# Optimization experiments

Measured on AMD Instinct MI355X. Metric: run time of the kernel, lower is better.

## Reference

```python
import jax, jax.numpy as jnp
import numpy as np

B, S, E, H = 2, 2048, 1024, 16
D = E // H

def setup_inputs() -> dict:
    key = jax.random.key(0)
    ks = jax.random.split(key, 11)
    sc = 0.02
    inp = {
        'queries': jax.random.normal(ks[0], (B, S, E), jnp.float32),
        'keys':    jax.random.normal(ks[1], (B, S, E), jnp.float32),
        'values':  jax.random.normal(ks[2], (B, S, E), jnp.float32),
        'Wq': jax.random.normal(ks[3], (E, E), jnp.float32) * sc,
        'bq': jnp.zeros((E,), jnp.float32),
        'Wk': jax.random.normal(ks[4], (E, E), jnp.float32) * sc,
        'bk': jnp.zeros((E,), jnp.float32),
        'Wv': jax.random.normal(ks[5], (E, E), jnp.float32) * sc,
        'bv': jnp.zeros((E,), jnp.float32),
        'Wo': jax.random.normal(ks[6], (E, E), jnp.float32) * sc,
        'bo': jnp.zeros((E,), jnp.float32),
        'indicator': 0,
    }
    return inp

def reference(queries, keys, values, Wq, bq, Wk, bk, Wv, bv, Wo, bo, indicator):
    # torch Linear: y = x @ W.T + b
    q = queries @ Wq.T + bq
    k = keys    @ Wk.T + bk
    v = values  @ Wv.T + bv
    # [B,S,E] -> [B,H,S,D]
    q = q.reshape(B, S, H, D).transpose(0, 2, 1, 3)
    k = k.reshape(B, S, H, D).transpose(0, 2, 1, 3)
    v = v.reshape(B, S, H, D).transpose(0, 2, 1, 3)
    scores = jnp.einsum('bhqd,bhkd->bhqk', q, k) / jnp.sqrt(jnp.float32(D))
    w = jax.nn.sigmoid(scores)
    if indicator != 0:
        w = 1.0 - w
    attn = jax.nn.softmax(w, axis=-1)  # dropout_prob=0 -> identity
    out = jnp.einsum('bhqk,bhkd->bhqd', attn, v)
    out = out.transpose(0, 2, 1, 3).reshape(B, S, E)
    return out @ Wo.T + bo
```

## Files before the change

kernel.cpp:

```cpp
#include <hip/hip_runtime.h>
#include <stdint.h>

#define Bb 2
#define Ss 2048
#define Ee 1024
#define Hh 16
#define Dd 64

typedef __bf16 bf16;
typedef __attribute__((ext_vector_type(8))) __bf16 bf16x8;
typedef __attribute__((ext_vector_type(4))) __bf16 bf16x4;
typedef __attribute__((ext_vector_type(4))) float f32x4;

#define MB (1u << 20)
#define OFF_XQ 0u
#define OFF_XK (8u * MB)
#define OFF_XV (16u * MB)
#define OFF_WQ (24u * MB)
#define OFF_WK (26u * MB)
#define OFF_WV (28u * MB)
#define OFF_WO (30u * MB)
#define OFF_Q  (32u * MB)
#define OFF_K  (40u * MB)
#define OFF_VT (48u * MB)
#define OFF_AO (56u * MB)

__device__ __forceinline__ void gll16(const void* g, void* lds) {
  __builtin_amdgcn_global_load_lds(
      (const __attribute__((address_space(1))) void*)g,
      (__attribute__((address_space(3))) void*)lds, 16, 0, 0);
}

__device__ __forceinline__ unsigned pkbf(float lo, float hi) {
  unsigned r;
  asm("v_cvt_pk_bf16_f32 %0, %1, %2" : "=v"(r) : "v"(lo), "v"(hi));
  return r;
}
#define PL32SWAP(a, b) asm("v_permlane32_swap_b32 %0, %1" : "+v"(a), "+v"(b))
#define PL16SWAP(a, b) asm("v_permlane16_swap_b32 %0, %1" : "+v"(a), "+v"(b))

__global__ __launch_bounds__(256) void convert_kernel(
    const float* __restrict__ q, const float* __restrict__ k, const float* __restrict__ v,
    const float* __restrict__ wq, const float* __restrict__ wk, const float* __restrict__ wv,
    const float* __restrict__ wo, const int* __restrict__ ind, char* __restrict__ ws)
{
  const unsigned i = blockIdx.x * 256u + threadIdx.x;
  const float* src;
  bf16* dst;
  float scale = 1.0f;
  if (i < 3145728u) {
    const unsigned a = i >> 20, j = i & 1048575u;
    src = (a == 0 ? q : a == 1 ? k : v) + (size_t)j * 4;
    dst = (bf16*)(ws + (size_t)a * (8u * MB)) + (size_t)j * 4;
  } else {
    const unsigned i2 = i - 3145728u;
    const unsigned a = i2 >> 18, j = i2 & 262143u;
    src = (a == 0 ? wq : a == 1 ? wk : a == 2 ? wv : wo) + (size_t)j * 4;
    dst = (bf16*)(ws + OFF_WQ + (size_t)a * (2u * MB)) + (size_t)j * 4;
    if (a == 0) {
      const float c1v = (*ind != 0) ? 1.442695041f : -1.442695041f;
      scale = 0.125f * c1v;
    }
  }
  const float4 f = *(const float4*)src;
  bf16x4 o;
  o[0] = (bf16)(f.x * scale);
  o[1] = (bf16)(f.y * scale);
  o[2] = (bf16)(f.z * scale);
  o[3] = (bf16)(f.w * scale);
  *(bf16x4*)dst = o;
}

__device__ __forceinline__ void gemm128_body(
    const bf16* __restrict__ A, const bf16* __restrict__ W,
    char* smem, int m0, int n0, int t, f32x4 (&acc)[4][4])
{
  char* As = smem;
  char* Bs = smem + 16384;
  const int lane = t & 63;
  const int wid = t >> 6;
  const int wm = (wid >> 1) << 6;
  const int wn = (wid & 1) << 6;
  for (int kt = 0; kt < 1024; kt += 64) {
    __syncthreads();
#pragma unroll
    for (int i = 0; i < 4; ++i) {
      const int L = i * 4096 + t * 16;
      const int r = L >> 7;
      const int c = ((L >> 4) & 7) ^ (r & 7);
      gll16(A + (size_t)(m0 + r) * 1024 + kt + c * 8, As + i * 4096 + wid * 1024);
      gll16(W + (size_t)(n0 + r) * 1024 + kt + c * 8, Bs + i * 4096 + wid * 1024);
    }
    __syncthreads();
#pragma unroll
    for (int ks = 0; ks < 2; ++ks) {
      bf16x8 af[4], bff[4];
#pragma unroll
      for (int mi = 0; mi < 4; ++mi) {
        const int r = wm + mi * 16 + (lane & 15);
        const int c = (ks * 4 + (lane >> 4)) ^ (r & 7);
        af[mi] = *(const bf16x8*)(As + r * 128 + c * 16);
      }
#pragma unroll
      for (int ni = 0; ni < 4; ++ni) {
        const int r = wn + ni * 16 + (lane & 15);
        const int c = (ks * 4 + (lane >> 4)) ^ (r & 7);
        bff[ni] = *(const bf16x8*)(Bs + r * 128 + c * 16);
      }
      __builtin_amdgcn_s_setprio(1);
#pragma unroll
      for (int mi = 0; mi < 4; ++mi)
#pragma unroll
        for (int ni = 0; ni < 4; ++ni)
          acc[mi][ni] = __builtin_amdgcn_mfma_f32_16x16x32_bf16(af[mi], bff[ni], acc[mi][ni], 0, 0, 0);
      __builtin_amdgcn_s_setprio(0);
    }
  }
}

__global__ __launch_bounds__(256) void proj_gemm(
    char* __restrict__ ws, const float* __restrict__ bq,
    const float* __restrict__ bk, const float* __restrict__ bv,
    const int* __restrict__ ind)
{
  __shared__ __align__(16) char smem[32768];
  const int zi = blockIdx.z;
  const bf16* A = (const bf16*)(ws + (zi == 0 ? OFF_XQ : zi == 1 ? OFF_XK : OFF_XV));
  const bf16* W = (const bf16*)(ws + (zi == 0 ? OFF_WQ : zi == 1 ? OFF_WK : OFF_WV));
  const float* bias = zi == 0 ? bq : zi == 1 ? bk : bv;
  bf16* outp = (bf16*)(ws + (zi == 0 ? OFF_Q : zi == 1 ? OFF_K : OFF_VT));
  const float c1v = (*ind != 0) ? 1.442695041f : -1.442695041f;
  const float bscale = (zi == 0) ? 0.125f * c1v : 1.0f;
  const int t = threadIdx.x;
  const int m0 = blockIdx.y * 128, n0 = blockIdx.x * 128;
  f32x4 acc[4][4] = {};
  gemm128_body(A, W, smem, m0, n0, t, acc);
  const int lane = t & 63, wid = t >> 6;
  const int wm = (wid >> 1) << 6, wn = (wid & 1) << 6;
  const int cl = lane & 15, rl = lane >> 4;
#pragma unroll
  for (int ni = 0; ni < 4; ++ni) {
    const int col = n0 + wn + ni * 16 + cl;
    const float bvv = bias[col] * bscale;
    const int h = col >> 6, d = col & 63;
#pragma unroll
    for (int mi = 0; mi < 4; ++mi) {
      const int row0 = m0 + wm + mi * 16 + rl * 4;
      const int b = row0 >> 11, s = row0 & 2047;
      if (zi == 2) {
        bf16x4 o;
#pragma unroll
        for (int r2 = 0; r2 < 4; ++r2) o[r2] = (bf16)(acc[mi][ni][r2] + bvv);
        *(bf16x4*)&outp[((size_t)((b * Hh + h) * Dd + d) * Ss) + s] = o;
      } else {
#pragma unroll
        for (int r2 = 0; r2 < 4; ++r2) {
          const float val = acc[mi][ni][r2] + bvv;
          outp[((size_t)((b * Hh + h) * Ss + s + r2) * Dd) + d] = (bf16)val;
        }
      }
    }
  }
}

__global__ __launch_bounds__(256, 2) void attn_kernel(char* __restrict__ ws)
{
  __shared__ __align__(16) char smem[49152];
  char* Qs  = smem;
  char* Ks  = smem + 16384;
  char* Vts = smem + 32768;
  char* Os  = smem;
  const int t = threadIdx.x, lane = t & 63, wid = t >> 6;
  const int g = lane >> 4, l15 = lane & 15;
  const int bh = blockIdx.y;
  const int q0 = blockIdx.x * 128;
  const bf16* Qg  = (const bf16*)(ws + OFF_Q)  + (size_t)bh * Ss * Dd;
  const bf16* Kg  = (const bf16*)(ws + OFF_K)  + (size_t)bh * Ss * Dd;
  const bf16* Vtg = (const bf16*)(ws + OFF_VT) + (size_t)bh * Ss * Dd;
  bf16* AO = (bf16*)(ws + OFF_AO);

#pragma unroll
  for (int i = 0; i < 4; ++i) {
    const int L = i * 4096 + t * 16;
    const int r = L >> 7;
    const int c = ((L >> 4) & 7) ^ (r & 7);
    gll16(Qg + (size_t)(q0 + r) * Dd + c * 8, Qs + i * 4096 + wid * 1024);
  }
  __syncthreads();
  bf16x8 qf[2][2];
#pragma unroll
  for (int qh = 0; qh < 2; ++qh)
#pragma unroll
    for (int ks = 0; ks < 2; ++ks) {
      const int r = wid * 32 + qh * 16 + l15;
      const int c = (ks * 4 + g) ^ (r & 7);
      qf[qh][ks] = *(const bf16x8*)(Qs + r * 128 + c * 16);
    }

  f32x4 acc_o[2][4] = {};
  f32x4 acc_sum[2] = {};
  union { unsigned u[4]; bf16x8 v; } ones_;
#pragma unroll
  for (int j = 0; j < 4; ++j) ones_.u[j] = 0x3F803F80u;

  for (int kt = 0; kt < Ss; kt += 128) {
    __syncthreads();
#pragma unroll
    for (int i = 0; i < 4; ++i) {
      const int L = i * 4096 + t * 16;
      const int r = L >> 7;
      const int c = ((L >> 4) & 7) ^ (r & 7);
      gll16(Kg + (size_t)(kt + r) * Dd + c * 8, Ks + i * 4096 + wid * 1024);
    }
#pragma unroll
    for (int i = 0; i < 4; ++i) {
      const int L = i * 4096 + t * 16;
      const int r = L >> 8;
      const int c = ((L >> 4) & 15) ^ (r & 15);
      gll16(Vtg + (size_t)r * Ss + kt + c * 8, Vts + i * 4096 + wid * 1024);
    }
    __syncthreads();

    f32x4 st[2][8];
#pragma unroll
    for (int qh = 0; qh < 2; ++qh)
#pragma unroll
      for (int ni = 0; ni < 8; ++ni)
        st[qh][ni] = (f32x4){-0.52876637f, -0.52876637f, -0.52876637f, -0.52876637f};
    __builtin_amdgcn_s_setprio(1);
#pragma unroll
    for (int ks = 0; ks < 2; ++ks) {
#pragma unroll
      for (int ni = 0; ni < 8; ++ni) {
        const int r = ni * 16 + l15;
        const int c = (ks * 4 + g) ^ (r & 7);
        const bf16x8 kf = *(const bf16x8*)(Ks + r * 128 + c * 16);
        st[0][ni] = __builtin_amdgcn_mfma_f32_16x16x32_bf16(kf, qf[0][ks], st[0][ni], 0, 0, 0);
        st[1][ni] = __builtin_amdgcn_mfma_f32_16x16x32_bf16(kf, qf[1][ks], st[1][ni], 0, 0, 0);
      }
    }
    __builtin_amdgcn_s_setprio(0);

#pragma unroll
    for (int kb = 0; kb < 4; ++kb) {
      union { unsigned u[4]; bf16x8 v; } pb[2];
#pragma unroll
      for (int qh = 0; qh < 2; ++qh) {
        float p[2][4];
#pragma unroll
        for (int e = 0; e < 2; ++e)
#pragma unroll
          for (int r2 = 0; r2 < 4; ++r2) {
            const float ex = __builtin_amdgcn_exp2f(st[qh][2 * kb + e][r2]);
            const float tt = __builtin_amdgcn_rcpf(0.69314718f + ex);
            p[e][r2] = __builtin_amdgcn_exp2f(tt);
          }
        unsigned E0 = pkbf(p[0][0], p[0][1]);
        unsigned E1 = pkbf(p[0][2], p[0][3]);
        unsigned O0 = pkbf(p[1][0], p[1][1]);
        unsigned O1 = pkbf(p[1][2], p[1][3]);
        PL32SWAP(E0, O0);
        PL16SWAP(E0, O0);
        PL32SWAP(E1, O1);
        PL16SWAP(E1, O1);
        pb[qh].u[0] = E0; pb[qh].u[1] = E1; pb[qh].u[2] = O0; pb[qh].u[3] = O1;
      }
      __builtin_amdgcn_s_setprio(1);
#pragma unroll
      for (int dblk = 0; dblk < 4; ++dblk) {
        const int r = dblk * 16 + l15;
        const int c = (kb * 4 + g) ^ (r & 15);
        const bf16x8 vf = *(const bf16x8*)(Vts + r * 256 + c * 16);
        acc_o[0][dblk] = __builtin_amdgcn_mfma_f32_16x16x32_bf16(vf, pb[0].v, acc_o[0][dblk], 0, 0, 0);
        acc_o[1][dblk] = __builtin_amdgcn_mfma_f32_16x16x32_bf16(vf, pb[1].v, acc_o[1][dblk], 0, 0, 0);
      }
      acc_sum[0] = __builtin_amdgcn_mfma_f32_16x16x32_bf16(ones_.v, pb[0].v, acc_sum[0], 0, 0, 0);
      acc_sum[1] = __builtin_amdgcn_mfma_f32_16x16x32_bf16(ones_.v, pb[1].v, acc_sum[1], 0, 0, 0);
      __builtin_amdgcn_s_setprio(0);
    }
  }

  const float rinv[2] = {__builtin_amdgcn_rcpf(acc_sum[0][0]),
                         __builtin_amdgcn_rcpf(acc_sum[1][0])};

  __syncthreads();
#pragma unroll
  for (int qh = 0; qh < 2; ++qh) {
    const int row = wid * 32 + qh * 16 + l15;
#pragma unroll
    for (int dblk = 0; dblk < 4; ++dblk) {
      const unsigned w0 = pkbf(acc_o[qh][dblk][0] * rinv[qh], acc_o[qh][dblk][1] * rinv[qh]);
      const unsigned w1 = pkbf(acc_o[qh][dblk][2] * rinv[qh], acc_o[qh][dblk][3] * rinv[qh]);
      const int cc = dblk * 2 + (g >> 1);
      char* a = Os + row * 128 + (cc ^ (row & 7)) * 16 + (g & 1) * 8;
      *(uint2*)a = make_uint2(w0, w1);
    }
  }
  __syncthreads();
  const int b = bh >> 4, h = bh & 15;
#pragma unroll
  for (int i = 0; i < 4; ++i) {
    const int L = i * 4096 + t * 16;
    const int r = L >> 7;
    const int cc = (L >> 4) & 7;
    const uint4 w = *(const uint4*)(Os + r * 128 + (cc ^ (r & 7)) * 16);
    *(uint4*)&AO[((size_t)(b * Ss + q0 + r) << 10) + h * 64 + cc * 8] = w;
  }
}

__global__ __launch_bounds__(256) void out_gemm(char* __restrict__ ws,
                                                const float* __restrict__ bo,
                                                float* __restrict__ outp)
{
  __shared__ __align__(16) char smem[24576];
  char* As = smem;
  char* Bs = smem + 16384;
  const bf16* A = (const bf16*)(ws + OFF_AO);
  const bf16* W = (const bf16*)(ws + OFF_WO);
  const int t = threadIdx.x, lane = t & 63, wid = t >> 6;
  const int l15 = lane & 15, g = lane >> 4;
  const int m0 = blockIdx.y * 128, n0 = blockIdx.x * 64;
  const int wm = (wid >> 1) << 6;
  const int wn = (wid & 1) << 5;
  f32x4 acc[4][2] = {};
  for (int kt = 0; kt < 1024; kt += 64) {
    __syncthreads();
#pragma unroll
    for (int i = 0; i < 4; ++i) {
      const int L = i * 4096 + t * 16;
      const int r = L >> 7;
      const int c = ((L >> 4) & 7) ^ (r & 7);
      gll16(A + (size_t)(m0 + r) * 1024 + kt + c * 8, As + i * 4096 + wid * 1024);
    }
#pragma unroll
    for (int i = 0; i < 2; ++i) {
      const int L = i * 4096 + t * 16;
      const int r = L >> 7;
      const int c = ((L >> 4) & 7) ^ (r & 7);
      gll16(W + (size_t)(n0 + r) * 1024 + kt + c * 8, Bs + i * 4096 + wid * 1024);
    }
    __syncthreads();
#pragma unroll
    for (int ks = 0; ks < 2; ++ks) {
      bf16x8 af[4], bff[2];
#pragma unroll
      for (int mi = 0; mi < 4; ++mi) {
        const int r = wm + mi * 16 + l15;
        const int c = (ks * 4 + g) ^ (r & 7);
        af[mi] = *(const bf16x8*)(As + r * 128 + c * 16);
      }
#pragma unroll
      for (int ni = 0; ni < 2; ++ni) {
        const int r = wn + ni * 16 + l15;
        const int c = (ks * 4 + g) ^ (r & 7);
        bff[ni] = *(const bf16x8*)(Bs + r * 128 + c * 16);
      }
      __builtin_amdgcn_s_setprio(1);
#pragma unroll
      for (int mi = 0; mi < 4; ++mi)
#pragma unroll
        for (int ni = 0; ni < 2; ++ni)
          acc[mi][ni] = __builtin_amdgcn_mfma_f32_16x16x32_bf16(af[mi], bff[ni], acc[mi][ni], 0, 0, 0);
      __builtin_amdgcn_s_setprio(0);
    }
  }
#pragma unroll
  for (int ni = 0; ni < 2; ++ni) {
    const int col = n0 + wn + ni * 16 + l15;
    const float bvv = bo[col];
#pragma unroll
    for (int mi = 0; mi < 4; ++mi)
#pragma unroll
      for (int r2 = 0; r2 < 4; ++r2) {
        const int row = m0 + wm + mi * 16 + g * 4 + r2;
        outp[(size_t)row * Ee + col] = acc[mi][ni][r2] + bvv;
      }
  }
}

extern "C" void kernel_launch(void* const* d_in, const int* in_sizes, int n_in,
                              void* d_out, int out_size, void* d_ws, size_t ws_size,
                              hipStream_t stream) {
  (void)in_sizes; (void)n_in; (void)out_size; (void)ws_size;
  const float* queries = (const float*)d_in[0];
  const float* keys    = (const float*)d_in[1];
  const float* values  = (const float*)d_in[2];
  const float* Wq = (const float*)d_in[3];
  const float* bq = (const float*)d_in[4];
  const float* Wk = (const float*)d_in[5];
  const float* bk = (const float*)d_in[6];
  const float* Wv = (const float*)d_in[7];
  const float* bv = (const float*)d_in[8];
  const float* Wo = (const float*)d_in[9];
  const float* bo = (const float*)d_in[10];
  const int* indicator = (const int*)d_in[11];
  char* ws = (char*)d_ws;
  float* outp = (float*)d_out;

  convert_kernel<<<16384, 256, 0, stream>>>(queries, keys, values, Wq, Wk, Wv, Wo, indicator, ws);
  proj_gemm<<<dim3(8, 32, 3), 256, 0, stream>>>(ws, bq, bk, bv, indicator);
  attn_kernel<<<dim3(16, 32), 256, 0, stream>>>(ws);
  out_gemm<<<dim3(16, 32), 256, 0, stream>>>(ws, bo, outp);
}
```

Before: 235.9 us.

## Shrink attention tile to 64 queries, swap MFMA operands for vector epilogues

The attention kernel now handles 64 query rows per block instead of 128. It loads Q fragments straight from global memory instead of staging them through LDS, cuts LDS to 32KB, raises launch bounds to 4 blocks per CU, and remaps a 1D grid so that neighbouring blocks share heads for L2 reuse. The Q/K projection and output GEMMs swap MFMA operands so each lane holds contiguous columns, which allows vectorized bf16x4/float4 stores and float4 bias loads instead of scattered scalar stores. The cost is that K/V tiles are loaded twice as many times in total for attention, with less MFMA work per K/V tile.

Measured after the change: 240.9 us. +2.1%, slower.

```diff
diff --git a/kernel.cpp b/kernel.cpp
--- a/kernel.cpp
+++ b/kernel.cpp
@@ -71,6 +71,7 @@
   *(bf16x4*)dst = o;
 }
 
+template <bool TR>
 __device__ __forceinline__ void gemm128_body(
     const bf16* __restrict__ A, const bf16* __restrict__ W,
     char* smem, int m0, int n0, int t, f32x4 (&acc)[4][4])
@@ -111,8 +112,12 @@
 #pragma unroll
       for (int mi = 0; mi < 4; ++mi)
 #pragma unroll
-        for (int ni = 0; ni < 4; ++ni)
-          acc[mi][ni] = __builtin_amdgcn_mfma_f32_16x16x32_bf16(af[mi], bff[ni], acc[mi][ni], 0, 0, 0);
+        for (int ni = 0; ni < 4; ++ni) {
+          if (TR)
+            acc[mi][ni] = __builtin_amdgcn_mfma_f32_16x16x32_bf16(bff[ni], af[mi], acc[mi][ni], 0, 0, 0);
+          else
+            acc[mi][ni] = __builtin_amdgcn_mfma_f32_16x16x32_bf16(af[mi], bff[ni], acc[mi][ni], 0, 0, 0);
+        }
       __builtin_amdgcn_s_setprio(0);
     }
   }
@@ -133,72 +138,72 @@
   const float bscale = (zi == 0) ? 0.125f * c1v : 1.0f;
   const int t = threadIdx.x;
   const int m0 = blockIdx.y * 128, n0 = blockIdx.x * 128;
-  f32x4 acc[4][4] = {};
-  gemm128_body(A, W, smem, m0, n0, t, acc);
   const int lane = t & 63, wid = t >> 6;
   const int wm = (wid >> 1) << 6, wn = (wid & 1) << 6;
-  const int cl = lane & 15, rl = lane >> 4;
-#pragma unroll
-  for (int ni = 0; ni < 4; ++ni) {
-    const int col = n0 + wn + ni * 16 + cl;
-    const float bvv = bias[col] * bscale;
-    const int h = col >> 6, d = col & 63;
-#pragma unroll
-    for (int mi = 0; mi < 4; ++mi) {
-      const int row0 = m0 + wm + mi * 16 + rl * 4;
-      const int b = row0 >> 11, s = row0 & 2047;
-      if (zi == 2) {
+  const int l15 = lane & 15, g = lane >> 4;
+  f32x4 acc[4][4] = {};
+  if (zi == 2) {
+    gemm128_body<false>(A, W, smem, m0, n0, t, acc);
+#pragma unroll
+    for (int ni = 0; ni < 4; ++ni) {
+      const int col = n0 + wn + ni * 16 + l15;
+      const float bvv = bias[col];
+      const int h = col >> 6, d = col & 63;
+#pragma unroll
+      for (int mi = 0; mi < 4; ++mi) {
+        const int row0 = m0 + wm + mi * 16 + g * 4;
+        const int b = row0 >> 11, s = row0 & 2047;
         bf16x4 o;
 #pragma unroll
         for (int r2 = 0; r2 < 4; ++r2) o[r2] = (bf16)(acc[mi][ni][r2] + bvv);
         *(bf16x4*)&outp[((size_t)((b * Hh + h) * Dd + d) * Ss) + s] = o;
-      } else {
-#pragma unroll
-        for (int r2 = 0; r2 < 4; ++r2) {
-          const float val = acc[mi][ni][r2] + bvv;
-          outp[((size_t)((b * Hh + h) * Ss + s + r2) * Dd) + d] = (bf16)val;
-        }
-      }
-    }
-  }
-}
-
-__global__ __launch_bounds__(256, 2) void attn_kernel(char* __restrict__ ws)
+      }
+    }
+  } else {
+    gemm128_body<true>(A, W, smem, m0, n0, t, acc);
+#pragma unroll
+    for (int mi = 0; mi < 4; ++mi) {
+      const int row = m0 + wm + mi * 16 + l15;
+      const int b = row >> 11, s = row & 2047;
+#pragma unroll
+      for (int ni = 0; ni < 4; ++ni) {
+        const int col0 = n0 + wn + ni * 16 + g * 4;
+        const int h = col0 >> 6, d0 = col0 & 63;
+        const float4 b4 = *(const float4*)&bias[col0];
+        bf16x4 o;
+        o[0] = (bf16)(acc[mi][ni][0] + b4.x * bscale);
+        o[1] = (bf16)(acc[mi][ni][1] + b4.y * bscale);
+        o[2] = (bf16)(acc[mi][ni][2] + b4.z * bscale);
+        o[3] = (bf16)(acc[mi][ni][3] + b4.w * bscale);
+        *(bf16x4*)&outp[((size_t)((b * Hh + h) * Ss + s) * Dd) + d0] = o;
+      }
+    }
+  }
+}
+
+__global__ __launch_bounds__(256, 4) void attn_kernel(char* __restrict__ ws)
 {
-  __shared__ __align__(16) char smem[49152];
-  char* Qs  = smem;
-  char* Ks  = smem + 16384;
-  char* Vts = smem + 32768;
+  __shared__ __align__(16) char smem[32768];
+  char* Ks  = smem;
+  char* Vts = smem + 16384;
   char* Os  = smem;
   const int t = threadIdx.x, lane = t & 63, wid = t >> 6;
   const int g = lane >> 4, l15 = lane & 15;
-  const int bh = blockIdx.y;
-  const int q0 = blockIdx.x * 128;
+  const int lin = blockIdx.x;
+  const int bh = ((lin & 7) << 2) + ((lin >> 3) & 3);
+  const int q0 = (lin >> 5) << 6;
   const bf16* Qg  = (const bf16*)(ws + OFF_Q)  + (size_t)bh * Ss * Dd;
   const bf16* Kg  = (const bf16*)(ws + OFF_K)  + (size_t)bh * Ss * Dd;
   const bf16* Vtg = (const bf16*)(ws + OFF_VT) + (size_t)bh * Ss * Dd;
   bf16* AO = (bf16*)(ws + OFF_AO);
 
-#pragma unroll
-  for (int i = 0; i < 4; ++i) {
-    const int L = i * 4096 + t * 16;
-    const int r = L >> 7;
-    const int c = ((L >> 4) & 7) ^ (r & 7);
-    gll16(Qg + (size_t)(q0 + r) * Dd + c * 8, Qs + i * 4096 + wid * 1024);
-  }
-  __syncthreads();
-  bf16x8 qf[2][2];
-#pragma unroll
-  for (int qh = 0; qh < 2; ++qh)
-#pragma unroll
-    for (int ks = 0; ks < 2; ++ks) {
-      const int r = wid * 32 + qh * 16 + l15;
-      const int c = (ks * 4 + g) ^ (r & 7);
-      qf[qh][ks] = *(const bf16x8*)(Qs + r * 128 + c * 16);
-    }
-
-  f32x4 acc_o[2][4] = {};
-  f32x4 acc_sum[2] = {};
+  bf16x8 qf[2];
+#pragma unroll
+  for (int ks = 0; ks < 2; ++ks)
+    qf[ks] = *(const bf16x8*)(Qg + (size_t)(q0 + wid * 16 + l15) * Dd + ks * 32 + g * 8);
+
+  f32x4 acc_o[4] = {};
+  f32x4 acc_sum = {};
   union { unsigned u[4]; bf16x8 v; } ones_;
 #pragma unroll
   for (int j = 0; j < 4; ++j) ones_.u[j] = 0x3F803F80u;
@@ -221,12 +226,10 @@
     }
     __syncthreads();
 
-    f32x4 st[2][8];
-#pragma unroll
-    for (int qh = 0; qh < 2; ++qh)
-#pragma unroll
-      for (int ni = 0; ni < 8; ++ni)
-        st[qh][ni] = (f32x4){-0.52876637f, -0.52876637f, -0.52876637f, -0.52876637f};
+    f32x4 st[8];
+#pragma unroll
+    for (int ni = 0; ni < 8; ++ni)
+      st[ni] = (f32x4){-0.52876637f, -0.52876637f, -0.52876637f, -0.52876637f};
     __builtin_amdgcn_s_setprio(1);
 #pragma unroll
     for (int ks = 0; ks < 2; ++ks) {
@@ -235,62 +238,54 @@
         const int r = ni * 16 + l15;
         const int c = (ks * 4 + g) ^ (r & 7);
         const bf16x8 kf = *(const bf16x8*)(Ks + r * 128 + c * 16);
-        st[0][ni] = __builtin_amdgcn_mfma_f32_16x16x32_bf16(kf, qf[0][ks], st[0][ni], 0, 0, 0);
-        st[1][ni] = __builtin_amdgcn_mfma_f32_16x16x32_bf16(kf, qf[1][ks], st[1][ni], 0, 0, 0);
+        st[ni] = __builtin_amdgcn_mfma_f32_16x16x32_bf16(kf, qf[ks], st[ni], 0, 0, 0);
       }
     }
     __builtin_amdgcn_s_setprio(0);
 
 #pragma unroll
     for (int kb = 0; kb < 4; ++kb) {
-      union { unsigned u[4]; bf16x8 v; } pb[2];
-#pragma unroll
-      for (int qh = 0; qh < 2; ++qh) {
-        float p[2][4];
-#pragma unroll
-        for (int e = 0; e < 2; ++e)
-#pragma unroll
-          for (int r2 = 0; r2 < 4; ++r2) {
-            const float ex = __builtin_amdgcn_exp2f(st[qh][2 * kb + e][r2]);
-            const float tt = __builtin_amdgcn_rcpf(0.69314718f + ex);
-            p[e][r2] = __builtin_amdgcn_exp2f(tt);
-          }
-        unsigned E0 = pkbf(p[0][0], p[0][1]);
-        unsigned E1 = pkbf(p[0][2], p[0][3]);
-        unsigned O0 = pkbf(p[1][0], p[1][1]);
-        unsigned O1 = pkbf(p[1][2], p[1][3]);
-        PL32SWAP(E0, O0);
-        PL16SWAP(E0, O0);
-        PL32SWAP(E1, O1);
-        PL16SWAP(E1, O1);
-        pb[qh].u[0] = E0; pb[qh].u[1] = E1; pb[qh].u[2] = O0; pb[qh].u[3] = O1;
-      }
+      float p[2][4];
+#pragma unroll
+      for (int e = 0; e < 2; ++e)
+#pragma unroll
+        for (int r2 = 0; r2 < 4; ++r2) {
+          const float ex = __builtin_amdgcn_exp2f(st[2 * kb + e][r2]);
+          const float tt = __builtin_amdgcn_rcpf(0.69314718f + ex);
+          p[e][r2] = __builtin_amdgcn_exp2f(tt);
+        }
+      unsigned E0 = pkbf(p[0][0], p[0][1]);
+      unsigned E1 = pkbf(p[0][2], p[0][3]);
+      unsigned O0 = pkbf(p[1][0], p[1][1]);
+      unsigned O1 = pkbf(p[1][2], p[1][3]);
+      PL32SWAP(E0, O0);
+      PL16SWAP(E0, O0);
+      PL32SWAP(E1, O1);
+      PL16SWAP(E1, O1);
+      union { unsigned u[4]; bf16x8 v; } pb;
+      pb.u[0] = E0; pb.u[1] = E1; pb.u[2] = O0; pb.u[3] = O1;
       __builtin_amdgcn_s_setprio(1);
 #pragma unroll
       for (int dblk = 0; dblk < 4; ++dblk) {
         const int r = dblk * 16 + l15;
         const int c = (kb * 4 + g) ^ (r & 15);
         const bf16x8 vf = *(const bf16x8*)(Vts + r * 256 + c * 16);
-        acc_o[0][dblk] = __builtin_amdgcn_mfma_f32_16x16x32_bf16(vf, pb[0].v, acc_o[0][dblk], 0, 0, 0);
-        acc_o[1][dblk] = __builtin_amdgcn_mfma_f32_16x16x32_bf16(vf, pb[1].v, acc_o[1][dblk], 0, 0, 0);
-      }
-      acc_sum[0] = __builtin_amdgcn_mfma_f32_16x16x32_bf16(ones_.v, pb[0].v, acc_sum[0], 0, 0, 0);
-      acc_sum[1] = __builtin_amdgcn_mfma_f32_16x16x32_bf16(ones_.v, pb[1].v, acc_sum[1], 0, 0, 0);
+        acc_o[dblk] = __builtin_amdgcn_mfma_f32_16x16x32_bf16(vf, pb.v, acc_o[dblk], 0, 0, 0);
+      }
+      acc_sum = __builtin_amdgcn_mfma_f32_16x16x32_bf16(ones_.v, pb.v, acc_sum, 0, 0, 0);
       __builtin_amdgcn_s_setprio(0);
     }
   }
 
-  const float rinv[2] = {__builtin_amdgcn_rcpf(acc_sum[0][0]),
-                         __builtin_amdgcn_rcpf(acc_sum[1][0])};
+  const float rinv = __builtin_amdgcn_rcpf(acc_sum[0]);
 
   __syncthreads();
-#pragma unroll
-  for (int qh = 0; qh < 2; ++qh) {
-    const int row = wid * 32 + qh * 16 + l15;
+  {
+    const int row = wid * 16 + l15;
 #pragma unroll
     for (int dblk = 0; dblk < 4; ++dblk) {
-      const unsigned w0 = pkbf(acc_o[qh][dblk][0] * rinv[qh], acc_o[qh][dblk][1] * rinv[qh]);
-      const unsigned w1 = pkbf(acc_o[qh][dblk][2] * rinv[qh], acc_o[qh][dblk][3] * rinv[qh]);
+      const unsigned w0 = pkbf(acc_o[dblk][0] * rinv, acc_o[dblk][1] * rinv);
+      const unsigned w1 = pkbf(acc_o[dblk][2] * rinv, acc_o[dblk][3] * rinv);
       const int cc = dblk * 2 + (g >> 1);
       char* a = Os + row * 128 + (cc ^ (row & 7)) * 16 + (g & 1) * 8;
       *(uint2*)a = make_uint2(w0, w1);
@@ -299,7 +294,7 @@
   __syncthreads();
   const int b = bh >> 4, h = bh & 15;
 #pragma unroll
-  for (int i = 0; i < 4; ++i) {
+  for (int i = 0; i < 2; ++i) {
     const int L = i * 4096 + t * 16;
     const int r = L >> 7;
     const int cc = (L >> 4) & 7;
@@ -360,21 +355,24 @@
       for (int mi = 0; mi < 4; ++mi)
 #pragma unroll
         for (int ni = 0; ni < 2; ++ni)
-          acc[mi][ni] = __builtin_amdgcn_mfma_f32_16x16x32_bf16(af[mi], bff[ni], acc[mi][ni], 0, 0, 0);
+          acc[mi][ni] = __builtin_amdgcn_mfma_f32_16x16x32_bf16(bff[ni], af[mi], acc[mi][ni], 0, 0, 0);
       __builtin_amdgcn_s_setprio(0);
     }
   }
 #pragma unroll
-  for (int ni = 0; ni < 2; ++ni) {
-    const int col = n0 + wn + ni * 16 + l15;
-    const float bvv = bo[col];
-#pragma unroll
-    for (int mi = 0; mi < 4; ++mi)
-#pragma unroll
-      for (int r2 = 0; r2 < 4; ++r2) {
-        const int row = m0 + wm + mi * 16 + g * 4 + r2;
-        outp[(size_t)row * Ee + col] = acc[mi][ni][r2] + bvv;
-      }
+  for (int mi = 0; mi < 4; ++mi) {
+    const int row = m0 + wm + mi * 16 + l15;
+#pragma unroll
+    for (int ni = 0; ni < 2; ++ni) {
+      const int col0 = n0 + wn + ni * 16 + g * 4;
+      const float4 b4 = *(const float4*)&bo[col0];
+      float4 o;
+      o.x = acc[mi][ni][0] + b4.x;
+      o.y = acc[mi][ni][1] + b4.y;
+      o.z = acc[mi][ni][2] + b4.z;
+      o.w = acc[mi][ni][3] + b4.w;
+      *(float4*)&outp[(size_t)row * Ee + col0] = o;
+    }
   }
 }
 
@@ -399,6 +397,6 @@
 
   convert_kernel<<<16384, 256, 0, stream>>>(queries, keys, values, Wq, Wk, Wv, Wo, indicator, ws);
   proj_gemm<<<dim3(8, 32, 3), 256, 0, stream>>>(ws, bq, bk, bv, indicator);
-  attn_kernel<<<dim3(16, 32), 256, 0, stream>>>(ws);
+  attn_kernel<<<1024, 256, 0, stream>>>(ws);
   out_gemm<<<dim3(16, 32), 256, 0, stream>>>(ws, bo, outp);
 }
```
